# Kernel optimization log

Measured on AMD Instinct MI355X. Metric: run time of the kernel, lower is better.

Reference implementation:

```python
import jax, jax.numpy as jnp
import numpy as np

N_ENTS = 50000
N_RELS2 = 460  # num_rels * 2
H_DIM = 128
T = 8
E = 200000
M = 400000
RRELU_SLOPE = (1.0 / 8.0 + 1.0 / 3.0) / 2.0  # F.rrelu eval mode
EPS = 1e-12


def l2norm(x):
    # F.normalize(x) along last dim
    return x / jnp.maximum(jnp.linalg.norm(x, axis=-1, keepdims=True), EPS)


def gru_cell(x, h, W_ih, W_hh, b_ih, b_hh):
    # torch.nn.GRUCell math
    gi = x @ W_ih.T + b_ih
    gh = h @ W_hh.T + b_hh
    i_r, i_z, i_n = jnp.split(gi, 3, axis=-1)
    h_r, h_z, h_n = jnp.split(gh, 3, axis=-1)
    r = jax.nn.sigmoid(i_r + h_r)
    z = jax.nn.sigmoid(i_z + h_z)
    n = jnp.tanh(i_n + r * h_n)
    return (1.0 - z) * n + z * h


def rrelu(x):
    return jnp.where(x >= 0, x, RRELU_SLOPE * x)


def setup_inputs() -> dict:
    key = jax.random.key(0)
    ks = jax.random.split(key, 12)
    src = jax.random.randint(ks[0], (T, E), 0, N_ENTS, dtype=jnp.int32)
    dst = jax.random.randint(ks[1], (T, E), 0, N_ENTS, dtype=jnp.int32)
    etype = jax.random.randint(ks[2], (T, E), 0, N_RELS2, dtype=jnp.int32)
    r_to_e_idx = jax.random.randint(ks[3], (T, M), 0, N_ENTS, dtype=jnp.int32)
    rel_seg = jax.random.randint(ks[4], (T, M), 0, N_RELS2, dtype=jnp.int32)
    s = 1.0 / np.sqrt(H_DIM)
    dynamic_emb = jax.random.normal(ks[5], (N_ENTS, H_DIM), jnp.float32)
    emb_rel = jax.random.normal(ks[6], (N_RELS2, H_DIM), jnp.float32) * s
    gru_W_ih = jax.random.uniform(ks[7], (3 * H_DIM, 2 * H_DIM), jnp.float32, -s, s)
    gru_W_hh = jax.random.uniform(ks[8], (3 * H_DIM, H_DIM), jnp.float32, -s, s)
    gru_b_ih = jnp.zeros((3 * H_DIM,), jnp.float32)
    gru_b_hh = jnp.zeros((3 * H_DIM,), jnp.float32)
    rgcn_W = jax.random.normal(ks[9], (2, H_DIM, H_DIM), jnp.float32) * s  # 2 hidden layers
    time_gate_weight = jax.random.normal(ks[10], (H_DIM, H_DIM), jnp.float32) * s
    time_gate_bias = jnp.zeros((H_DIM,), jnp.float32)
    return {
        "src": src, "dst": dst, "etype": etype,
        "r_to_e_idx": r_to_e_idx, "rel_seg": rel_seg,
        "dynamic_emb": dynamic_emb, "emb_rel": emb_rel,
        "gru_W_ih": gru_W_ih, "gru_W_hh": gru_W_hh,
        "gru_b_ih": gru_b_ih, "gru_b_hh": gru_b_hh,
        "rgcn_W": rgcn_W,
        "time_gate_weight": time_gate_weight, "time_gate_bias": time_gate_bias,
    }


def reference(src, dst, etype, r_to_e_idx, rel_seg, dynamic_emb, emb_rel,
              gru_W_ih, gru_W_hh, gru_b_ih, gru_b_hh, rgcn_W,
              time_gate_weight, time_gate_bias):
    h_init = l2norm(dynamic_emb)  # layer_norm=True path

    def step(carry, xs):
        h, h0 = carry
        src_t, dst_t, etype_t, rte_t, rseg_t = xs
        # --- relation evolution: mean of incident entity embeddings per relation ---
        temp_e = h[rte_t]  # [M, d]
        sums = jax.ops.segment_sum(temp_e, rseg_t, num_segments=N_RELS2)
        cnts = jax.ops.segment_sum(jnp.ones((M,), h.dtype), rseg_t, num_segments=N_RELS2)
        x_mean = jnp.where(cnts[:, None] > 0, sums / jnp.maximum(cnts[:, None], 1.0), 0.0)
        x_input = jnp.concatenate([emb_rel, x_mean], axis=1)  # [2R, 2d]
        h0 = l2norm(gru_cell(x_input, h0, gru_W_ih, gru_W_hh, gru_b_ih, gru_b_hh))
        # --- RGCN (UnionRGCNLayer x2): msg=(h[src]+r[etype])@W, sum agg, 1/indeg norm, rrelu ---
        deg = jax.ops.segment_sum(jnp.ones((E,), h.dtype), dst_t, num_segments=N_ENTS)
        norm = jnp.where(deg > 0, 1.0 / jnp.maximum(deg, 1.0), 0.0)  # [N]
        nh = h
        for l in range(2):
            msg = (nh[src_t] + h0[etype_t]) @ rgcn_W[l]  # [E, d]
            agg = jax.ops.segment_sum(msg, dst_t, num_segments=N_ENTS) * norm[:, None]
            nh = rrelu(agg)
        current_h = l2norm(nh)
        # --- time gate fusion ---
        tw = jax.nn.sigmoid(h @ time_gate_weight + time_gate_bias)
        h_new = tw * current_h + (1.0 - tw) * h
        return (h_new, h0), h_new

    (_, h0_final), history = jax.lax.scan(
        step, (h_init, emb_rel), (src, dst, etype, r_to_e_idx, rel_seg))
    return history, h0_final  # [T, N, d], [2R, d]
```

## Files before the change

### kernel.cpp

```cpp
#include <hip/hip_runtime.h>
#include <math.h>

#define NENT 50000
#define NR2 460
#define HD 128
#define TS 8
#define EPC 200000
#define MPC 400000
#define RSLOPE 0.22916666666666666f
#define RBLK 128
#define NTOT (TS * NENT)
#define NB8 ((NTOT + 255) / 256)
#define SCAN2_PER ((NB8 + 255) / 256)
#define RSP 8

typedef __attribute__((ext_vector_type(8))) short bfrag;
typedef __attribute__((ext_vector_type(4))) float facc;

__device__ __forceinline__ float sigm(float x) { return 1.0f / (1.0f + expf(-x)); }
__device__ __forceinline__ float rrelu_f(float x) { return x >= 0.0f ? x : RSLOPE * x; }
__device__ __forceinline__ unsigned short f2bf_rne(float x) {
  unsigned u = __float_as_uint(x);
  unsigned r = (u + 0x7FFFu + ((u >> 16) & 1u)) >> 16;
  return (unsigned short)r;
}
__device__ __forceinline__ float bf2f(unsigned short b) {
  return __uint_as_float(((unsigned)b) << 16);
}
__device__ __forceinline__ float bfLO(unsigned u) { return __uint_as_float(u << 16); }
__device__ __forceinline__ float bfHI(unsigned u) { return __uint_as_float(u & 0xFFFF0000u); }

__global__ __launch_bounds__(HD) void k_l2rows(const float* __restrict__ in,
                                               float* __restrict__ out,
                                               unsigned short* __restrict__ out_bf) {
  int r = blockIdx.x, j = threadIdx.x;
  __shared__ float red[HD];
  float v = in[(size_t)r * HD + j];
  red[j] = v * v;
  __syncthreads();
  for (int s = HD / 2; s > 0; s >>= 1) { if (j < s) red[j] += red[j + s]; __syncthreads(); }
  float rn = 1.0f / fmaxf(sqrtf(red[0]), 1e-12f);
  float o = v * rn;
  out[(size_t)r * HD + j] = o;
  out_bf[(size_t)r * HD + j] = f2bf_rne(o);
}

__global__ void k_hist(const int* __restrict__ idx, int* __restrict__ cnt,
                       int n, int per_t, int stride) {
  int i = blockIdx.x * blockDim.x + threadIdx.x;
  int gs = gridDim.x * blockDim.x;
  for (; i < n; i += gs) atomicAdd(&cnt[(i / per_t) * stride + idx[i]], 1);
}

__global__ __launch_bounds__(256) void k_histR2(const int* __restrict__ rseg,
                                                int* __restrict__ blkcnt) {
  __shared__ int h[NR2];
  int b = blockIdx.x, t = blockIdx.y, tid = threadIdx.x;
  for (int i = tid; i < NR2; i += 256) h[i] = 0;
  __syncthreads();
  const int* rs = rseg + (size_t)t * MPC;
  int chunk = (MPC + RBLK - 1) / RBLK;
  int m0 = b * chunk, m1 = min(MPC, m0 + chunk);
  for (int m = m0 + tid; m < m1; m += 256) atomicAdd(&h[rs[m]], 1);
  __syncthreads();
  for (int i = tid; i < NR2; i += 256) blkcnt[((size_t)(t * RBLK + b)) * NR2 + i] = h[i];
}

__global__ __launch_bounds__(256) void k_scanR2a(const int* __restrict__ blkcnt,
                                                 int* __restrict__ tot) {
  int idx = blockIdx.x * 256 + threadIdx.x;
  if (idx >= TS * NR2) return;
  int t = idx / NR2, r = idx - t * NR2;
  int s = 0;
  for (int b = 0; b < RBLK; ++b) s += blkcnt[((size_t)(t * RBLK + b)) * NR2 + r];
  tot[idx] = s;
}

__global__ __launch_bounds__(512) void k_scanR2b(const int* __restrict__ tot,
    int* __restrict__ offsR, float* __restrict__ invc) {
  __shared__ int s[TS * NR2];
  int tid = threadIdx.x;
  for (int i = tid; i < TS * NR2; i += 512) s[i] = tot[i];
  __syncthreads();
  if (tid < TS) {
    int acc = tid * MPC;
    for (int r = 0; r < NR2; ++r) { int c = s[tid * NR2 + r]; s[tid * NR2 + r] = acc; acc += c; }
  }
  __syncthreads();
  for (int i = tid; i < TS * NR2; i += 512) {
    offsR[i] = s[i];
    int c = tot[i];
    invc[i] = c > 0 ? 1.0f / (float)c : 0.0f;
  }
  if (tid == 0) offsR[TS * NR2] = TS * MPC;
}

__global__ __launch_bounds__(256) void k_scanR2c(int* __restrict__ blkcnt,
                                                 const int* __restrict__ offsR) {
  int gw = (blockIdx.x * blockDim.x + threadIdx.x) >> 6;
  int lane = threadIdx.x & 63;
  if (gw >= TS * NR2) return;
  int t = gw / NR2, r = gw - t * NR2;
  size_t i0 = ((size_t)(t * RBLK + lane * 2)) * NR2 + r;
  size_t i1 = ((size_t)(t * RBLK + lane * 2 + 1)) * NR2 + r;
  int v0 = blkcnt[i0], v1 = blkcnt[i1];
  int s = v0 + v1;
  int sc = s;
  #pragma unroll
  for (int o = 1; o < 64; o <<= 1) {
    int x = __shfl_up(sc, o, 64);
    if (lane >= o) sc += x;
  }
  int basev = offsR[gw] + (sc - s);
  blkcnt[i0] = basev;
  blkcnt[i1] = basev + v0;
}

__global__ __launch_bounds__(256) void k_scatterR2(const int* __restrict__ rte,
    const int* __restrict__ rseg, const int* __restrict__ blkbase,
    int* __restrict__ out) {
  __shared__ int cur[NR2];
  int b = blockIdx.x, t = blockIdx.y, tid = threadIdx.x;
  for (int i = tid; i < NR2; i += 256) cur[i] = blkbase[((size_t)(t * RBLK + b)) * NR2 + i];
  __syncthreads();
  const int* rs = rseg + (size_t)t * MPC;
  const int* re = rte + (size_t)t * MPC;
  int chunk = (MPC + RBLK - 1) / RBLK;
  int m0 = b * chunk, m1 = min(MPC, m0 + chunk);
  for (int m = m0 + tid; m < m1; m += 256) {
    int r = rs[m];
    int p = atomicAdd(&cur[r], 1);
    out[p] = re[m];
  }
}

__global__ __launch_bounds__(256) void k_scan1(const int* __restrict__ deg,
    int* __restrict__ offs, float* __restrict__ normv, int* __restrict__ bsum) {
  __shared__ int sd[256];
  int b = blockIdx.x, tid = threadIdx.x;
  int i = b * 256 + tid;
  int v = (i < NTOT) ? deg[i] : 0;
  sd[tid] = v;
  __syncthreads();
  for (int o = 1; o < 256; o <<= 1) {
    int x = (tid >= o) ? sd[tid - o] : 0;
    __syncthreads();
    sd[tid] += x;
    __syncthreads();
  }
  if (i < NTOT) {
    offs[i] = sd[tid] - v;
    normv[i] = v > 0 ? 1.0f / (float)v : 0.0f;
  }
  if (tid == 255) bsum[b] = sd[255];
}

__global__ __launch_bounds__(256) void k_scan2(int* __restrict__ bsum) {
  __shared__ int part[256];
  int tid = threadIdx.x;
  int base = tid * SCAN2_PER;
  int local[SCAN2_PER];
  int s = 0;
  #pragma unroll
  for (int k = 0; k < SCAN2_PER; ++k) {
    int v = (base + k < NB8) ? bsum[base + k] : 0;
    local[k] = s;
    s += v;
  }
  part[tid] = s;
  __syncthreads();
  for (int o = 1; o < 256; o <<= 1) {
    int x = (tid >= o) ? part[tid - o] : 0;
    __syncthreads();
    part[tid] += x;
    __syncthreads();
  }
  int pre = (tid > 0) ? part[tid - 1] : 0;
  #pragma unroll
  for (int k = 0; k < SCAN2_PER; ++k)
    if (base + k < NB8) bsum[base + k] = pre + local[k];
}

__global__ __launch_bounds__(256) void k_scan3(int* __restrict__ offs, int* __restrict__ cur,
                                               const int* __restrict__ bsum) {
  int b = blockIdx.x;
  int i = b * 256 + threadIdx.x;
  if (i < NTOT) {
    int o = offs[i] + bsum[b];
    offs[i] = o;
    cur[i] = o;
  }
  if (b == 0 && threadIdx.x == 0) offs[NTOT] = TS * EPC;
}

__global__ void k_scatterE(const int* __restrict__ src, const int* __restrict__ dst,
                           const int* __restrict__ ety, int* __restrict__ cur,
                           unsigned* __restrict__ se) {
  int i = blockIdx.x * blockDim.x + threadIdx.x;
  int gs = gridDim.x * blockDim.x;
  for (; i < TS * EPC; i += gs) {
    int t = i / EPC;
    int d = dst[i];
    int p = atomicAdd(&cur[t * NENT + d], 1);
    se[p] = ((unsigned)src[i] << 9) | (unsigned)ety[i];
  }
}

__global__ __launch_bounds__(256) void k_prepW(const float* __restrict__ W,
    unsigned short* __restrict__ hi, unsigned short* __restrict__ lo) {
  int t = blockIdx.x * 256 + threadIdx.x;
  int nt = t >> 8, ks = (t >> 6) & 3, lane = t & 63;
  int n = nt * 16 + (lane & 15);
  int k0 = ks * 32 + ((lane >> 4) << 3);
  #pragma unroll
  for (int j = 0; j < 8; ++j) {
    float v = W[(k0 + j) * HD + n];
    unsigned short h = f2bf_rne(v);
    hi[t * 8 + j] = h;
    lo[t * 8 + j] = f2bf_rne(v - bf2f(h));
  }
}

__global__ __launch_bounds__(256) void k_relmean(const unsigned short* __restrict__ h_bf,
    const int* __restrict__ offs, const int* __restrict__ rte_csr,
    float* __restrict__ partials) {
  int rel = blockIdx.x, sp = blockIdx.y;
  int o0 = offs[rel], o1 = offs[rel + 1];
  int n = o1 - o0;
  int w = __builtin_amdgcn_readfirstlane(threadIdx.x >> 6);
  int lane = threadIdx.x & 63;
  int s0 = o0 + ((n * sp) >> 3);
  int s1 = o0 + ((n * (sp + 1)) >> 3);
  const unsigned* h4 = (const unsigned*)h_bf;
  float sx = 0.f, sy = 0.f;
  int p = s0 + w;
  for (; p + 12 < s1; p += 16) {
    int i0 = rte_csr[p];
    int i1 = rte_csr[p + 4];
    int i2 = rte_csr[p + 8];
    int i3 = rte_csr[p + 12];
    unsigned u0 = h4[(size_t)i0 * 64 + lane];
    unsigned u1 = h4[(size_t)i1 * 64 + lane];
    unsigned u2 = h4[(size_t)i2 * 64 + lane];
    unsigned u3 = h4[(size_t)i3 * 64 + lane];
    sx += (bfLO(u0) + bfLO(u1)) + (bfLO(u2) + bfLO(u3));
    sy += (bfHI(u0) + bfHI(u1)) + (bfHI(u2) + bfHI(u3));
  }
  for (; p < s1; p += 4) {
    unsigned u0 = h4[(size_t)rte_csr[p] * 64 + lane];
    sx += bfLO(u0);
    sy += bfHI(u0);
  }
  __shared__ float red[4][HD];
  red[w][lane * 2] = sx;
  red[w][lane * 2 + 1] = sy;
  __syncthreads();
  if (threadIdx.x < HD) {
    int j = threadIdx.x;
    float t = red[0][j] + red[1][j] + red[2][j] + red[3][j];
    partials[((size_t)sp * NR2 + rel) * HD + j] = t;
  }
}

__global__ __launch_bounds__(HD) void k_gru(
    const float* __restrict__ partials, const float* __restrict__ invcnt,
    const float* __restrict__ emb_rel, const float* __restrict__ h0s,
    const float* __restrict__ Wih, const float* __restrict__ Whh,
    const float* __restrict__ bih, const float* __restrict__ bhh,
    float* __restrict__ h0d) {
  int r = blockIdx.x, j = threadIdx.x;
  __shared__ __align__(16) float xr[2 * HD];
  __shared__ __align__(16) float hh[HD];
  __shared__ float red[HD];
  float inv = invcnt[r];
  xr[j] = emb_rel[r * HD + j];
  float xm = 0.f;
  #pragma unroll
  for (int sp = 0; sp < RSP; ++sp) xm += partials[((size_t)sp * NR2 + r) * HD + j];
  xr[HD + j] = xm * inv;
  float hv0 = h0s[r * HD + j];
  hh[j] = hv0;
  __syncthreads();
  float gr = bih[j], gz = bih[HD + j], gn = bih[2 * HD + j];
  const float4* W4 = (const float4*)Wih;
  int rowA = j * 64, rowB = (j + HD) * 64, rowC = (j + 2 * HD) * 64;
  #pragma unroll 4
  for (int k4 = 0; k4 < 64; ++k4) {
    float4 xa = ((const float4*)xr)[k4];
    float4 w0 = W4[rowA + k4];
    float4 w1 = W4[rowB + k4];
    float4 w2 = W4[rowC + k4];
    gr += w0.x * xa.x + w0.y * xa.y + w0.z * xa.z + w0.w * xa.w;
    gz += w1.x * xa.x + w1.y * xa.y + w1.z * xa.z + w1.w * xa.w;
    gn += w2.x * xa.x + w2.y * xa.y + w2.z * xa.z + w2.w * xa.w;
  }
  float hr = bhh[j], hz = bhh[HD + j], hn = bhh[2 * HD + j];
  const float4* Wh4 = (const float4*)Whh;
  int rA = j * 32, rB = (j + HD) * 32, rC = (j + 2 * HD) * 32;
  #pragma unroll 4
  for (int k4 = 0; k4 < 32; ++k4) {
    float4 xa = ((const float4*)hh)[k4];
    float4 w0 = Wh4[rA + k4];
    float4 w1 = Wh4[rB + k4];
    float4 w2 = Wh4[rC + k4];
    hr += w0.x * xa.x + w0.y * xa.y + w0.z * xa.z + w0.w * xa.w;
    hz += w1.x * xa.x + w1.y * xa.y + w1.z * xa.z + w1.w * xa.w;
    hn += w2.x * xa.x + w2.y * xa.y + w2.z * xa.z + w2.w * xa.w;
  }
  float rg = sigm(gr + hr);
  float zg = sigm(gz + hz);
  float ng = tanhf(gn + rg * hn);
  float hv = (1.0f - zg) * ng + zg * hv0;
  red[j] = hv * hv;
  __syncthreads();
  for (int s = HD / 2; s > 0; s >>= 1) { if (j < s) red[j] += red[j + s]; __syncthreads(); }
  float rn = 1.0f / fmaxf(sqrtf(red[0]), 1e-12f);
  h0d[r * HD + j] = hv * rn;
}

__global__ __launch_bounds__(256) void k_edge_csr(
    const unsigned short* __restrict__ nh_bf, const float* __restrict__ h0,
    const int* __restrict__ offs, const unsigned* __restrict__ se,
    const float* __restrict__ norm, float* __restrict__ agg) {
  int gw = __builtin_amdgcn_readfirstlane((blockIdx.x * blockDim.x + threadIdx.x) >> 6);
  int lane = threadIdx.x & 63;
  if (gw >= NENT) return;
  int o0 = offs[gw], o1 = offs[gw + 1];
  const unsigned* nh4 = (const unsigned*)nh_bf;
  const float2* h02 = (const float2*)h0;
  float sx = 0.f, sy = 0.f;
  int p = o0;
  for (; p + 4 <= o1; p += 4) {
    unsigned e0 = se[p], e1 = se[p + 1], e2 = se[p + 2], e3 = se[p + 3];
    unsigned ua = nh4[(size_t)(e0 >> 9) * 64 + lane];
    unsigned ub = nh4[(size_t)(e1 >> 9) * 64 + lane];
    unsigned uc = nh4[(size_t)(e2 >> 9) * 64 + lane];
    unsigned ud = nh4[(size_t)(e3 >> 9) * 64 + lane];
    float2 ra = h02[(size_t)(e0 & 511u) * 64 + lane];
    float2 rb = h02[(size_t)(e1 & 511u) * 64 + lane];
    float2 rc = h02[(size_t)(e2 & 511u) * 64 + lane];
    float2 rd = h02[(size_t)(e3 & 511u) * 64 + lane];
    sx += ((bfLO(ua) + ra.x) + (bfLO(ub) + rb.x)) +
          ((bfLO(uc) + rc.x) + (bfLO(ud) + rd.x));
    sy += ((bfHI(ua) + ra.y) + (bfHI(ub) + rb.y)) +
          ((bfHI(uc) + rc.y) + (bfHI(ud) + rd.y));
  }
  if (p + 2 <= o1) {
    unsigned e0 = se[p], e1 = se[p + 1];
    unsigned ua = nh4[(size_t)(e0 >> 9) * 64 + lane];
    unsigned ub = nh4[(size_t)(e1 >> 9) * 64 + lane];
    float2 ra = h02[(size_t)(e0 & 511u) * 64 + lane];
    float2 rb = h02[(size_t)(e1 & 511u) * 64 + lane];
    sx += (bfLO(ua) + ra.x) + (bfLO(ub) + rb.x);
    sy += (bfHI(ua) + ra.y) + (bfHI(ub) + rb.y);
    p += 2;
  }
  if (p < o1) {
    unsigned e0 = se[p];
    unsigned ua = nh4[(size_t)(e0 >> 9) * 64 + lane];
    float2 ra = h02[(size_t)(e0 & 511u) * 64 + lane];
    sx += bfLO(ua) + ra.x;
    sy += bfHI(ua) + ra.y;
  }
  float nm = norm[gw];
  ((float2*)agg)[(size_t)gw * 64 + lane] = make_float2(sx * nm, sy * nm);
}

__device__ __forceinline__ void stage_rows(const float* __restrict__ A, int base, int nrows,
                                           unsigned short* AsH, unsigned short* AsL,
                                           int tid) {
  const float4* A4 = (const float4*)A;
  #pragma unroll
  for (int it = 0; it < 8; ++it) {
    int idx = tid + it * 256;
    int r = idx >> 5, c4 = idx & 31;
    int c0 = c4 * 4;
    float4 v = make_float4(0.f, 0.f, 0.f, 0.f);
    if (base + r < nrows) v = A4[(size_t)(base + r) * 32 + c4];
    int chunk = (c0 >> 3) ^ (r & 7);
    int p = r * 128 + chunk * 8 + (c0 & 7);
    unsigned short h0 = f2bf_rne(v.x), h1 = f2bf_rne(v.y);
    unsigned short h2 = f2bf_rne(v.z), h3 = f2bf_rne(v.w);
    ushort4 hv; hv.x = h0; hv.y = h1; hv.z = h2; hv.w = h3;
    *(ushort4*)&AsH[p] = hv;
    ushort4 lv;
    lv.x = f2bf_rne(v.x - bf2f(h0)); lv.y = f2bf_rne(v.y - bf2f(h1));
    lv.z = f2bf_rne(v.z - bf2f(h2)); lv.w = f2bf_rne(v.w - bf2f(h3));
    *(ushort4*)&AsL[p] = lv;
  }
}

__device__ __forceinline__ void mfma_128(const unsigned short* AsH, const unsigned short* AsL,
                                         const unsigned short* __restrict__ wHi,
                                         const unsigned short* __restrict__ wLo,
                                         int w, int lane, facc* acc) {
  int lrow = lane & 15;
  int arow = w * 16 + lrow;
  #pragma unroll
  for (int ks = 0; ks < 4; ++ks) {
    int chunk = (ks * 4 + (lane >> 4)) ^ (arow & 7);
    int p = arow * 128 + chunk * 8;
    bfrag aH = *(const bfrag*)&AsH[p];
    bfrag aL = *(const bfrag*)&AsL[p];
    #pragma unroll
    for (int nt = 0; nt < 8; ++nt) {
      int fi = ((nt * 4 + ks) * 64 + lane) * 8;
      bfrag bH = *(const bfrag*)&wHi[fi];
      bfrag bL = *(const bfrag*)&wLo[fi];
      acc[nt] = __builtin_amdgcn_mfma_f32_16x16x32_bf16(aH, bH, acc[nt], 0, 0, 0);
      acc[nt] = __builtin_amdgcn_mfma_f32_16x16x32_bf16(aH, bL, acc[nt], 0, 0, 0);
      acc[nt] = __builtin_amdgcn_mfma_f32_16x16x32_bf16(aL, bH, acc[nt], 0, 0, 0);
    }
  }
}

__global__ __launch_bounds__(256) void k_mm1(
    const float* __restrict__ A, unsigned short* __restrict__ Abf,
    const unsigned short* __restrict__ wHi, const unsigned short* __restrict__ wLo,
    int nrows) {
  __shared__ __align__(16) unsigned short AsH[64 * 128];
  __shared__ __align__(16) unsigned short AsL[64 * 128];
  int tid = threadIdx.x;
  int base = blockIdx.x * 64;
  stage_rows(A, base, nrows, AsH, AsL, tid);
  __syncthreads();
  int w = tid >> 6, lane = tid & 63;
  int lrow = lane & 15, lk = lane >> 4;
  facc acc[8];
  #pragma unroll
  for (int nt = 0; nt < 8; ++nt) acc[nt] = (facc){0.f, 0.f, 0.f, 0.f};
  mfma_128(AsH, AsL, wHi, wLo, w, lane, acc);
  #pragma unroll
  for (int nt = 0; nt < 8; ++nt)
    #pragma unroll
    for (int r = 0; r < 4; ++r) {
      int row = base + w * 16 + lk * 4 + r;
      if (row < nrows) Abf[(size_t)row * HD + nt * 16 + lrow] = f2bf_rne(rrelu_f(acc[nt][r]));
    }
}

__global__ __launch_bounds__(256) void k_mm2_final(
    const float* __restrict__ A, const float* __restrict__ Hin,
    float* __restrict__ Hout, unsigned short* __restrict__ Hout_bf,
    const unsigned short* __restrict__ w2Hi, const unsigned short* __restrict__ w2Lo,
    const unsigned short* __restrict__ wtHi, const unsigned short* __restrict__ wtLo,
    const float* __restrict__ bias, int nrows) {
  __shared__ __align__(16) unsigned short AsH[64 * 128];
  __shared__ __align__(16) unsigned short AsL[64 * 128];
  int tid = threadIdx.x;
  int base = blockIdx.x * 64;
  int w = tid >> 6, lane = tid & 63;
  int lrow = lane & 15, lk = lane >> 4;
  stage_rows(A, base, nrows, AsH, AsL, tid);
  __syncthreads();
  facc acc[8];
  #pragma unroll
  for (int nt = 0; nt < 8; ++nt) acc[nt] = (facc){0.f, 0.f, 0.f, 0.f};
  mfma_128(AsH, AsL, w2Hi, w2Lo, w, lane, acc);
  #pragma unroll
  for (int nt = 0; nt < 8; ++nt)
    #pragma unroll
    for (int r = 0; r < 4; ++r) acc[nt][r] = rrelu_f(acc[nt][r]);
  __syncthreads();
  stage_rows(Hin, base, nrows, AsH, AsL, tid);
  __syncthreads();
  facc acc2[8];
  #pragma unroll
  for (int nt = 0; nt < 8; ++nt) acc2[nt] = (facc){0.f, 0.f, 0.f, 0.f};
  mfma_128(AsH, AsL, wtHi, wtLo, w, lane, acc2);
  float ss[4] = {0.f, 0.f, 0.f, 0.f};
  #pragma unroll
  for (int r = 0; r < 4; ++r) {
    #pragma unroll
    for (int nt = 0; nt < 8; ++nt) ss[r] += acc[nt][r] * acc[nt][r];
    #pragma unroll
    for (int o = 1; o < 16; o <<= 1) ss[r] += __shfl_xor(ss[r], o, 64);
    ss[r] = 1.0f / fmaxf(sqrtf(ss[r]), 1e-12f);
  }
  #pragma unroll
  for (int r = 0; r < 4; ++r) {
    int row = base + w * 16 + lk * 4 + r;
    if (row >= nrows) continue;
    #pragma unroll
    for (int nt = 0; nt < 8; ++nt) {
      int col = nt * 16 + lrow;
      float hv = Hin[(size_t)row * HD + col];
      float tw = sigm(acc2[nt][r] + bias[col]);
      float res = tw * (acc[nt][r] * ss[r]) + (1.0f - tw) * hv;
      Hout[(size_t)row * HD + col] = res;
      Hout_bf[(size_t)row * HD + col] = f2bf_rne(res);
    }
  }
}

extern "C" void kernel_launch(void* const* d_in, const int* in_sizes, int n_in,
                              void* d_out, int out_size, void* d_ws, size_t ws_size,
                              hipStream_t stream) {
  const int* src    = (const int*)d_in[0];
  const int* dst    = (const int*)d_in[1];
  const int* etype  = (const int*)d_in[2];
  const int* rte    = (const int*)d_in[3];
  const int* rseg   = (const int*)d_in[4];
  const float* dyn  = (const float*)d_in[5];
  const float* emb_rel = (const float*)d_in[6];
  const float* W_ih = (const float*)d_in[7];
  const float* W_hh = (const float*)d_in[8];
  const float* b_ih = (const float*)d_in[9];
  const float* b_hh = (const float*)d_in[10];
  const float* rgcnW = (const float*)d_in[11];
  const float* tgW  = (const float*)d_in[12];
  const float* tgB  = (const float*)d_in[13];
  float* out = (float*)d_out;
  (void)in_sizes; (void)n_in; (void)out_size; (void)ws_size;

  float* ws = (float*)d_ws;
  size_t off = 0;
  float* agg1    = ws + off; off += (size_t)NENT * HD;
  float* agg2    = ws + off; off += (size_t)NENT * HD;
  float* parts   = ws + off; off += (size_t)RSP * NR2 * HD;
  float* h0a     = ws + off; off += (size_t)NR2 * HD;
  float* h0b     = ws + off; off += (size_t)NR2 * HD;
  float* normv8  = ws + off; off += NTOT;
  float* invc8   = ws + off; off += TS * NR2;
  off = (off + 3) & ~(size_t)3;
  unsigned short* h_bf    = (unsigned short*)(ws + off); off += (size_t)NENT * HD / 2;
  unsigned short* agg1_bf = (unsigned short*)(ws + off); off += (size_t)NENT * HD / 2;
  unsigned short* wf = (unsigned short*)(ws + off);
  unsigned short* w1H = wf;            unsigned short* w1L = wf + 16384;
  unsigned short* w2H = wf + 32768;    unsigned short* w2L = wf + 49152;
  unsigned short* wtH = wf + 65536;    unsigned short* wtL = wf + 81920;
  off += (6 * 16384) / 2;
  unsigned* csr_se8 = (unsigned*)(ws + off); off += (size_t)TS * EPC;
  int* csr_rte8  = (int*)(ws + off);  off += (size_t)TS * MPC;
  int* degE8     = (int*)(ws + off);  off += NTOT;
  int* offsE8    = (int*)(ws + off);  off += NTOT + 2;
  int* curE8     = (int*)(ws + off);  off += NTOT;
  int* bsum      = (int*)(ws + off);  off += NB8;
  int* blkcntR8  = (int*)(ws + off);  off += (size_t)TS * RBLK * NR2;
  int* offsR8    = (int*)(ws + off);  off += TS * NR2 + 2;
  int* totR      = (int*)(ws + off);  off += TS * NR2;

  hipMemsetAsync(degE8, 0, (size_t)NTOT * sizeof(int), stream);
  k_hist<<<2048, 256, 0, stream>>>(dst, degE8, TS * EPC, EPC, NENT);
  k_scan1<<<NB8, 256, 0, stream>>>(degE8, offsE8, normv8, bsum);
  k_scan2<<<1, 256, 0, stream>>>(bsum);
  k_scan3<<<NB8, 256, 0, stream>>>(offsE8, curE8, bsum);
  k_scatterE<<<2048, 256, 0, stream>>>(src, dst, etype, curE8, csr_se8);
  k_histR2<<<dim3(RBLK, TS), 256, 0, stream>>>(rseg, blkcntR8);
  k_scanR2a<<<(TS * NR2 + 255) / 256, 256, 0, stream>>>(blkcntR8, totR);
  k_scanR2b<<<1, 512, 0, stream>>>(totR, offsR8, invc8);
  k_scanR2c<<<(TS * NR2 * 64 + 255) / 256, 256, 0, stream>>>(blkcntR8, offsR8);
  k_scatterR2<<<dim3(RBLK, TS), 256, 0, stream>>>(rte, rseg, blkcntR8, csr_rte8);
  k_prepW<<<8, 256, 0, stream>>>(rgcnW, w1H, w1L);
  k_prepW<<<8, 256, 0, stream>>>(rgcnW + HD * HD, w2H, w2L);
  k_prepW<<<8, 256, 0, stream>>>(tgW, wtH, wtL);

  k_l2rows<<<NENT, HD, 0, stream>>>(dyn, out, h_bf);

  float* h0bufs[2] = {h0a, h0b};
  for (int t = 0; t < TS; ++t) {
    const float* h = out + (size_t)(t == 0 ? 0 : (t - 1)) * NENT * HD;
    float* hout = out + (size_t)t * NENT * HD;
    const float* h0s = (t == 0) ? emb_rel : h0bufs[(t - 1) & 1];
    float* h0d = h0bufs[t & 1];

    k_relmean<<<dim3(NR2, RSP), 256, 0, stream>>>(h_bf, offsR8 + t * NR2, csr_rte8, parts);
    k_gru<<<NR2, HD, 0, stream>>>(parts, invc8 + t * NR2, emb_rel, h0s,
                                  W_ih, W_hh, b_ih, b_hh, h0d);

    k_edge_csr<<<(NENT * 64 + 255) / 256, 256, 0, stream>>>(
        h_bf, h0d, offsE8 + t * NENT, csr_se8, normv8 + t * NENT, agg1);
    k_mm1<<<(NENT + 63) / 64, 256, 0, stream>>>(agg1, agg1_bf, w1H, w1L, NENT);
    k_edge_csr<<<(NENT * 64 + 255) / 256, 256, 0, stream>>>(
        agg1_bf, h0d, offsE8 + t * NENT, csr_se8, normv8 + t * NENT, agg2);
    k_mm2_final<<<(NENT + 63) / 64, 256, 0, stream>>>(agg2, h, hout, h_bf,
                                                      w2H, w2L, wtH, wtL, tgB, NENT);
  }
  hipMemcpyAsync(out + (size_t)TS * NENT * HD, h0bufs[(TS - 1) & 1],
                 (size_t)NR2 * HD * sizeof(float), hipMemcpyDeviceToDevice, stream);
}
```

Measured before the change: 1.561 ms.

## Fuse relation mean with GRU, cache relation sums, and pair rows per wave in edge aggregation

Merges the relation-mean and GRU kernels into one 512-thread block per relation, which drops the partials buffer and one launch per step. The edge aggregation now has each wave process two destination rows so that more gathers are in flight. The first pass computes the per-node relation-embedding sum from a bf16 copy of h0 and stores it as bf16, and the second pass reuses that stored sum instead of gathering it again. The cost is bf16 rounding of h0 and of the cached sum, an imbalance when the two rows have different degrees, and a scatter kernel that now loops per timestep with a smaller grid.

```diff
diff --git a/kernel.cpp b/kernel.cpp
--- a/kernel.cpp
+++ b/kernel.cpp
@@ -2,6 +2,7 @@
 #include <math.h>
 
 #define NENT 50000
+#define NE2 (NENT / 2)
 #define NR2 460
 #define HD 128
 #define TS 8
@@ -12,7 +13,6 @@
 #define NTOT (TS * NENT)
 #define NB8 ((NTOT + 255) / 256)
 #define SCAN2_PER ((NB8 + 255) / 256)
-#define RSP 8
 
 typedef __attribute__((ext_vector_type(8))) short bfrag;
 typedef __attribute__((ext_vector_type(4))) float facc;
@@ -29,6 +29,9 @@
 }
 __device__ __forceinline__ float bfLO(unsigned u) { return __uint_as_float(u << 16); }
 __device__ __forceinline__ float bfHI(unsigned u) { return __uint_as_float(u & 0xFFFF0000u); }
+__device__ __forceinline__ unsigned packbf(float x, float y) {
+  return (unsigned)f2bf_rne(x) | ((unsigned)f2bf_rne(y) << 16);
+}
 
 __global__ __launch_bounds__(HD) void k_l2rows(const float* __restrict__ in,
                                                float* __restrict__ out,
@@ -196,13 +199,18 @@
 __global__ void k_scatterE(const int* __restrict__ src, const int* __restrict__ dst,
                            const int* __restrict__ ety, int* __restrict__ cur,
                            unsigned* __restrict__ se) {
-  int i = blockIdx.x * blockDim.x + threadIdx.x;
+  int tid0 = blockIdx.x * blockDim.x + threadIdx.x;
   int gs = gridDim.x * blockDim.x;
-  for (; i < TS * EPC; i += gs) {
-    int t = i / EPC;
-    int d = dst[i];
-    int p = atomicAdd(&cur[t * NENT + d], 1);
-    se[p] = ((unsigned)src[i] << 9) | (unsigned)ety[i];
+  for (int t = 0; t < TS; ++t) {
+    const int* s = src + (size_t)t * EPC;
+    const int* d = dst + (size_t)t * EPC;
+    const int* e = ety + (size_t)t * EPC;
+    int* ct = cur + t * NENT;
+    for (int i = tid0; i < EPC; i += gs) {
+      int dd = d[i];
+      int p = atomicAdd(&ct[dd], 1);
+      se[p] = ((unsigned)s[i] << 9) | (unsigned)e[i];
+    }
   }
 }
 
@@ -221,24 +229,27 @@
   }
 }
 
-__global__ __launch_bounds__(256) void k_relmean(const unsigned short* __restrict__ h_bf,
+__global__ __launch_bounds__(512) void k_relgru(
+    const unsigned short* __restrict__ h_bf,
     const int* __restrict__ offs, const int* __restrict__ rte_csr,
-    float* __restrict__ partials) {
-  int rel = blockIdx.x, sp = blockIdx.y;
+    const float* __restrict__ invcnt,
+    const float* __restrict__ emb_rel, const float* __restrict__ h0s,
+    const float* __restrict__ Wih, const float* __restrict__ Whh,
+    const float* __restrict__ bih, const float* __restrict__ bhh,
+    float* __restrict__ h0d, unsigned short* __restrict__ h0d_bf) {
+  int rel = blockIdx.x;
+  int tid = threadIdx.x;
+  int w = __builtin_amdgcn_readfirstlane(tid >> 6);
+  int lane = tid & 63;
   int o0 = offs[rel], o1 = offs[rel + 1];
   int n = o1 - o0;
-  int w = __builtin_amdgcn_readfirstlane(threadIdx.x >> 6);
-  int lane = threadIdx.x & 63;
-  int s0 = o0 + ((n * sp) >> 3);
-  int s1 = o0 + ((n * (sp + 1)) >> 3);
+  int s0 = o0 + ((n * w) >> 3);
+  int s1 = o0 + ((n * (w + 1)) >> 3);
   const unsigned* h4 = (const unsigned*)h_bf;
   float sx = 0.f, sy = 0.f;
-  int p = s0 + w;
-  for (; p + 12 < s1; p += 16) {
-    int i0 = rte_csr[p];
-    int i1 = rte_csr[p + 4];
-    int i2 = rte_csr[p + 8];
-    int i3 = rte_csr[p + 12];
+  int p = s0;
+  for (; p + 4 <= s1; p += 4) {
+    int i0 = rte_csr[p], i1 = rte_csr[p + 1], i2 = rte_csr[p + 2], i3 = rte_csr[p + 3];
     unsigned u0 = h4[(size_t)i0 * 64 + lane];
     unsigned u1 = h4[(size_t)i1 * 64 + lane];
     unsigned u2 = h4[(size_t)i2 * 64 + lane];
@@ -246,124 +257,162 @@
     sx += (bfLO(u0) + bfLO(u1)) + (bfLO(u2) + bfLO(u3));
     sy += (bfHI(u0) + bfHI(u1)) + (bfHI(u2) + bfHI(u3));
   }
-  for (; p < s1; p += 4) {
+  for (; p < s1; ++p) {
     unsigned u0 = h4[(size_t)rte_csr[p] * 64 + lane];
     sx += bfLO(u0);
     sy += bfHI(u0);
   }
-  __shared__ float red[4][HD];
+  __shared__ float red[8][HD];
   red[w][lane * 2] = sx;
   red[w][lane * 2 + 1] = sy;
   __syncthreads();
-  if (threadIdx.x < HD) {
-    int j = threadIdx.x;
-    float t = red[0][j] + red[1][j] + red[2][j] + red[3][j];
-    partials[((size_t)sp * NR2 + rel) * HD + j] = t;
-  }
-}
-
-__global__ __launch_bounds__(HD) void k_gru(
-    const float* __restrict__ partials, const float* __restrict__ invcnt,
-    const float* __restrict__ emb_rel, const float* __restrict__ h0s,
-    const float* __restrict__ Wih, const float* __restrict__ Whh,
-    const float* __restrict__ bih, const float* __restrict__ bhh,
-    float* __restrict__ h0d) {
-  int r = blockIdx.x, j = threadIdx.x;
   __shared__ __align__(16) float xr[2 * HD];
   __shared__ __align__(16) float hh[HD];
-  __shared__ float red[HD];
-  float inv = invcnt[r];
-  xr[j] = emb_rel[r * HD + j];
-  float xm = 0.f;
-  #pragma unroll
-  for (int sp = 0; sp < RSP; ++sp) xm += partials[((size_t)sp * NR2 + r) * HD + j];
-  xr[HD + j] = xm * inv;
-  float hv0 = h0s[r * HD + j];
-  hh[j] = hv0;
-  __syncthreads();
-  float gr = bih[j], gz = bih[HD + j], gn = bih[2 * HD + j];
-  const float4* W4 = (const float4*)Wih;
-  int rowA = j * 64, rowB = (j + HD) * 64, rowC = (j + 2 * HD) * 64;
-  #pragma unroll 4
-  for (int k4 = 0; k4 < 64; ++k4) {
-    float4 xa = ((const float4*)xr)[k4];
-    float4 w0 = W4[rowA + k4];
-    float4 w1 = W4[rowB + k4];
-    float4 w2 = W4[rowC + k4];
-    gr += w0.x * xa.x + w0.y * xa.y + w0.z * xa.z + w0.w * xa.w;
-    gz += w1.x * xa.x + w1.y * xa.y + w1.z * xa.z + w1.w * xa.w;
-    gn += w2.x * xa.x + w2.y * xa.y + w2.z * xa.z + w2.w * xa.w;
-  }
-  float hr = bhh[j], hz = bhh[HD + j], hn = bhh[2 * HD + j];
-  const float4* Wh4 = (const float4*)Whh;
-  int rA = j * 32, rB = (j + HD) * 32, rC = (j + 2 * HD) * 32;
-  #pragma unroll 4
-  for (int k4 = 0; k4 < 32; ++k4) {
-    float4 xa = ((const float4*)hh)[k4];
-    float4 w0 = Wh4[rA + k4];
-    float4 w1 = Wh4[rB + k4];
-    float4 w2 = Wh4[rC + k4];
-    hr += w0.x * xa.x + w0.y * xa.y + w0.z * xa.z + w0.w * xa.w;
-    hz += w1.x * xa.x + w1.y * xa.y + w1.z * xa.z + w1.w * xa.w;
-    hn += w2.x * xa.x + w2.y * xa.y + w2.z * xa.z + w2.w * xa.w;
-  }
-  float rg = sigm(gr + hr);
-  float zg = sigm(gz + hz);
-  float ng = tanhf(gn + rg * hn);
-  float hv = (1.0f - zg) * ng + zg * hv0;
-  red[j] = hv * hv;
-  __syncthreads();
-  for (int s = HD / 2; s > 0; s >>= 1) { if (j < s) red[j] += red[j + s]; __syncthreads(); }
-  float rn = 1.0f / fmaxf(sqrtf(red[0]), 1e-12f);
-  h0d[r * HD + j] = hv * rn;
-}
-
-__global__ __launch_bounds__(256) void k_edge_csr(
-    const unsigned short* __restrict__ nh_bf, const float* __restrict__ h0,
+  __shared__ float red2[HD];
+  float hv0 = 0.f;
+  if (tid < HD) {
+    int j = tid;
+    float inv = invcnt[rel];
+    float xm = 0.f;
+    #pragma unroll
+    for (int sp = 0; sp < 8; ++sp) xm += red[sp][j];
+    xr[j] = emb_rel[rel * HD + j];
+    xr[HD + j] = xm * inv;
+    hv0 = h0s[rel * HD + j];
+    hh[j] = hv0;
+  }
+  __syncthreads();
+  float hv = 0.f;
+  if (tid < HD) {
+    int j = tid;
+    float gr = bih[j], gz = bih[HD + j], gn = bih[2 * HD + j];
+    const float4* W4 = (const float4*)Wih;
+    int rowA = j * 64, rowB = (j + HD) * 64, rowC = (j + 2 * HD) * 64;
+    #pragma unroll 4
+    for (int k4 = 0; k4 < 64; ++k4) {
+      float4 xa = ((const float4*)xr)[k4];
+      float4 w0 = W4[rowA + k4];
+      float4 w1 = W4[rowB + k4];
+      float4 w2 = W4[rowC + k4];
+      gr += w0.x * xa.x + w0.y * xa.y + w0.z * xa.z + w0.w * xa.w;
+      gz += w1.x * xa.x + w1.y * xa.y + w1.z * xa.z + w1.w * xa.w;
+      gn += w2.x * xa.x + w2.y * xa.y + w2.z * xa.z + w2.w * xa.w;
+    }
+    float hr = bhh[j], hz = bhh[HD + j], hn = bhh[2 * HD + j];
+    const float4* Wh4 = (const float4*)Whh;
+    int rA = j * 32, rB = (j + HD) * 32, rC = (j + 2 * HD) * 32;
+    #pragma unroll 4
+    for (int k4 = 0; k4 < 32; ++k4) {
+      float4 xa = ((const float4*)hh)[k4];
+      float4 w0 = Wh4[rA + k4];
+      float4 w1 = Wh4[rB + k4];
+      float4 w2 = Wh4[rC + k4];
+      hr += w0.x * xa.x + w0.y * xa.y + w0.z * xa.z + w0.w * xa.w;
+      hz += w1.x * xa.x + w1.y * xa.y + w1.z * xa.z + w1.w * xa.w;
+      hn += w2.x * xa.x + w2.y * xa.y + w2.z * xa.z + w2.w * xa.w;
+    }
+    float rg = sigm(gr + hr);
+    float zg = sigm(gz + hz);
+    float ng = tanhf(gn + rg * hn);
+    hv = (1.0f - zg) * ng + zg * hv0;
+    red2[tid] = hv * hv;
+  }
+  __syncthreads();
+  for (int s = HD / 2; s > 0; s >>= 1) {
+    if (tid < s) red2[tid] += red2[tid + s];
+    __syncthreads();
+  }
+  if (tid < HD) {
+    float rn = 1.0f / fmaxf(sqrtf(red2[0]), 1e-12f);
+    float o = hv * rn;
+    h0d[rel * HD + tid] = o;
+    h0d_bf[rel * HD + tid] = f2bf_rne(o);
+  }
+}
+
+template<int PASS>
+__global__ __launch_bounds__(256) void k_edge2(
+    const unsigned short* __restrict__ nh_bf, const unsigned short* __restrict__ h0_bf,
     const int* __restrict__ offs, const unsigned* __restrict__ se,
-    const float* __restrict__ norm, float* __restrict__ agg) {
+    const float* __restrict__ norm, unsigned* __restrict__ Tbf,
+    float* __restrict__ agg) {
   int gw = __builtin_amdgcn_readfirstlane((blockIdx.x * blockDim.x + threadIdx.x) >> 6);
   int lane = threadIdx.x & 63;
-  if (gw >= NENT) return;
-  int o0 = offs[gw], o1 = offs[gw + 1];
+  if (gw >= NE2) return;
+  int rA = gw, rB = gw + NE2;
+  int a0 = offs[rA], a1 = offs[rA + 1];
+  int b0 = offs[rB], b1 = offs[rB + 1];
   const unsigned* nh4 = (const unsigned*)nh_bf;
-  const float2* h02 = (const float2*)h0;
-  float sx = 0.f, sy = 0.f;
-  int p = o0;
-  for (; p + 4 <= o1; p += 4) {
-    unsigned e0 = se[p], e1 = se[p + 1], e2 = se[p + 2], e3 = se[p + 3];
+  const unsigned* h04 = (const unsigned*)h0_bf;
+  float nax = 0.f, nay = 0.f, tax = 0.f, tay = 0.f;
+  float nbx = 0.f, nby = 0.f, tbx = 0.f, tby = 0.f;
+  int pa = a0, pb = b0;
+  for (; pa + 4 <= a1 && pb + 4 <= b1; pa += 4, pb += 4) {
+    unsigned e0 = se[pa], e1 = se[pa + 1], e2 = se[pa + 2], e3 = se[pa + 3];
+    unsigned f0 = se[pb], f1 = se[pb + 1], f2 = se[pb + 2], f3 = se[pb + 3];
     unsigned ua = nh4[(size_t)(e0 >> 9) * 64 + lane];
     unsigned ub = nh4[(size_t)(e1 >> 9) * 64 + lane];
     unsigned uc = nh4[(size_t)(e2 >> 9) * 64 + lane];
     unsigned ud = nh4[(size_t)(e3 >> 9) * 64 + lane];
-    float2 ra = h02[(size_t)(e0 & 511u) * 64 + lane];
-    float2 rb = h02[(size_t)(e1 & 511u) * 64 + lane];
-    float2 rc = h02[(size_t)(e2 & 511u) * 64 + lane];
-    float2 rd = h02[(size_t)(e3 & 511u) * 64 + lane];
-    sx += ((bfLO(ua) + ra.x) + (bfLO(ub) + rb.x)) +
-          ((bfLO(uc) + rc.x) + (bfLO(ud) + rd.x));
-    sy += ((bfHI(ua) + ra.y) + (bfHI(ub) + rb.y)) +
-          ((bfHI(uc) + rc.y) + (bfHI(ud) + rd.y));
-  }
-  if (p + 2 <= o1) {
-    unsigned e0 = se[p], e1 = se[p + 1];
+    unsigned va = nh4[(size_t)(f0 >> 9) * 64 + lane];
+    unsigned vb = nh4[(size_t)(f1 >> 9) * 64 + lane];
+    unsigned vc = nh4[(size_t)(f2 >> 9) * 64 + lane];
+    unsigned vd = nh4[(size_t)(f3 >> 9) * 64 + lane];
+    nax += (bfLO(ua) + bfLO(ub)) + (bfLO(uc) + bfLO(ud));
+    nay += (bfHI(ua) + bfHI(ub)) + (bfHI(uc) + bfHI(ud));
+    nbx += (bfLO(va) + bfLO(vb)) + (bfLO(vc) + bfLO(vd));
+    nby += (bfHI(va) + bfHI(vb)) + (bfHI(vc) + bfHI(vd));
+    if (PASS == 1) {
+      unsigned ha = h04[(size_t)(e0 & 511u) * 64 + lane];
+      unsigned hb = h04[(size_t)(e1 & 511u) * 64 + lane];
+      unsigned hc = h04[(size_t)(e2 & 511u) * 64 + lane];
+      unsigned hd = h04[(size_t)(e3 & 511u) * 64 + lane];
+      unsigned ga = h04[(size_t)(f0 & 511u) * 64 + lane];
+      unsigned gb = h04[(size_t)(f1 & 511u) * 64 + lane];
+      unsigned gc = h04[(size_t)(f2 & 511u) * 64 + lane];
+      unsigned gd = h04[(size_t)(f3 & 511u) * 64 + lane];
+      tax += (bfLO(ha) + bfLO(hb)) + (bfLO(hc) + bfLO(hd));
+      tay += (bfHI(ha) + bfHI(hb)) + (bfHI(hc) + bfHI(hd));
+      tbx += (bfLO(ga) + bfLO(gb)) + (bfLO(gc) + bfLO(gd));
+      tby += (bfHI(ga) + bfHI(gb)) + (bfHI(gc) + bfHI(gd));
+    }
+  }
+  for (; pa < a1; ++pa) {
+    unsigned e0 = se[pa];
     unsigned ua = nh4[(size_t)(e0 >> 9) * 64 + lane];
-    unsigned ub = nh4[(size_t)(e1 >> 9) * 64 + lane];
-    float2 ra = h02[(size_t)(e0 & 511u) * 64 + lane];
-    float2 rb = h02[(size_t)(e1 & 511u) * 64 + lane];
-    sx += (bfLO(ua) + ra.x) + (bfLO(ub) + rb.x);
-    sy += (bfHI(ua) + ra.y) + (bfHI(ub) + rb.y);
-    p += 2;
-  }
-  if (p < o1) {
-    unsigned e0 = se[p];
-    unsigned ua = nh4[(size_t)(e0 >> 9) * 64 + lane];
-    float2 ra = h02[(size_t)(e0 & 511u) * 64 + lane];
-    sx += bfLO(ua) + ra.x;
-    sy += bfHI(ua) + ra.y;
-  }
-  float nm = norm[gw];
-  ((float2*)agg)[(size_t)gw * 64 + lane] = make_float2(sx * nm, sy * nm);
+    nax += bfLO(ua);
+    nay += bfHI(ua);
+    if (PASS == 1) {
+      unsigned ha = h04[(size_t)(e0 & 511u) * 64 + lane];
+      tax += bfLO(ha);
+      tay += bfHI(ha);
+    }
+  }
+  for (; pb < b1; ++pb) {
+    unsigned f0 = se[pb];
+    unsigned va = nh4[(size_t)(f0 >> 9) * 64 + lane];
+    nbx += bfLO(va);
+    nby += bfHI(va);
+    if (PASS == 1) {
+      unsigned ga = h04[(size_t)(f0 & 511u) * 64 + lane];
+      tbx += bfLO(ga);
+      tby += bfHI(ga);
+    }
+  }
+  float nma = norm[rA], nmb = norm[rB];
+  if (PASS == 1) {
+    Tbf[(size_t)rA * 64 + lane] = packbf(tax, tay);
+    Tbf[(size_t)rB * 64 + lane] = packbf(tbx, tby);
+    ((float2*)agg)[(size_t)rA * 64 + lane] = make_float2((nax + tax) * nma, (nay + tay) * nma);
+    ((float2*)agg)[(size_t)rB * 64 + lane] = make_float2((nbx + tbx) * nmb, (nby + tby) * nmb);
+  } else {
+    unsigned tva = Tbf[(size_t)rA * 64 + lane];
+    unsigned tvb = Tbf[(size_t)rB * 64 + lane];
+    ((float2*)agg)[(size_t)rA * 64 + lane] =
+        make_float2((nax + bfLO(tva)) * nma, (nay + bfHI(tva)) * nma);
+    ((float2*)agg)[(size_t)rB * 64 + lane] =
+        make_float2((nbx + bfLO(tvb)) * nmb, (nby + bfHI(tvb)) * nmb);
+  }
 }
 
 __device__ __forceinline__ void stage_rows(const float* __restrict__ A, int base, int nrows,
@@ -517,14 +566,16 @@
   size_t off = 0;
   float* agg1    = ws + off; off += (size_t)NENT * HD;
   float* agg2    = ws + off; off += (size_t)NENT * HD;
-  float* parts   = ws + off; off += (size_t)RSP * NR2 * HD;
   float* h0a     = ws + off; off += (size_t)NR2 * HD;
   float* h0b     = ws + off; off += (size_t)NR2 * HD;
   float* normv8  = ws + off; off += NTOT;
   float* invc8   = ws + off; off += TS * NR2;
   off = (off + 3) & ~(size_t)3;
+  unsigned* Tbf  = (unsigned*)(ws + off); off += (size_t)NENT * 64;
   unsigned short* h_bf    = (unsigned short*)(ws + off); off += (size_t)NENT * HD / 2;
   unsigned short* agg1_bf = (unsigned short*)(ws + off); off += (size_t)NENT * HD / 2;
+  unsigned short* h0abf   = (unsigned short*)(ws + off); off += (size_t)NR2 * HD / 2 + 1;
+  unsigned short* h0bbf   = (unsigned short*)(ws + off); off += (size_t)NR2 * HD / 2 + 1;
   unsigned short* wf = (unsigned short*)(ws + off);
   unsigned short* w1H = wf;            unsigned short* w1L = wf + 16384;
   unsigned short* w2H = wf + 32768;    unsigned short* w2L = wf + 49152;
@@ -545,7 +596,7 @@
   k_scan1<<<NB8, 256, 0, stream>>>(degE8, offsE8, normv8, bsum);
   k_scan2<<<1, 256, 0, stream>>>(bsum);
   k_scan3<<<NB8, 256, 0, stream>>>(offsE8, curE8, bsum);
-  k_scatterE<<<2048, 256, 0, stream>>>(src, dst, etype, curE8, csr_se8);
+  k_scatterE<<<1024, 256, 0, stream>>>(src, dst, etype, curE8, csr_se8);
   k_histR2<<<dim3(RBLK, TS), 256, 0, stream>>>(rseg, blkcntR8);
   k_scanR2a<<<(TS * NR2 + 255) / 256, 256, 0, stream>>>(blkcntR8, totR);
   k_scanR2b<<<1, 512, 0, stream>>>(totR, offsR8, invc8);
@@ -558,21 +609,24 @@
   k_l2rows<<<NENT, HD, 0, stream>>>(dyn, out, h_bf);
 
   float* h0bufs[2] = {h0a, h0b};
+  unsigned short* h0bfbufs[2] = {h0abf, h0bbf};
   for (int t = 0; t < TS; ++t) {
     const float* h = out + (size_t)(t == 0 ? 0 : (t - 1)) * NENT * HD;
     float* hout = out + (size_t)t * NENT * HD;
     const float* h0s = (t == 0) ? emb_rel : h0bufs[(t - 1) & 1];
     float* h0d = h0bufs[t & 1];
-
-    k_relmean<<<dim3(NR2, RSP), 256, 0, stream>>>(h_bf, offsR8 + t * NR2, csr_rte8, parts);
-    k_gru<<<NR2, HD, 0, stream>>>(parts, invc8 + t * NR2, emb_rel, h0s,
-                                  W_ih, W_hh, b_ih, b_hh, h0d);
-
-    k_edge_csr<<<(NENT * 64 + 255) / 256, 256, 0, stream>>>(
-        h_bf, h0d, offsE8 + t * NENT, csr_se8, normv8 + t * NENT, agg1);
+    unsigned short* h0d_bf = h0bfbufs[t & 1];
+
+    k_relgru<<<NR2, 512, 0, stream>>>(h_bf, offsR8 + t * NR2, csr_rte8,
+                                      invc8 + t * NR2, emb_rel, h0s,
+                                      W_ih, W_hh, b_ih, b_hh, h0d, h0d_bf);
+
+    k_edge2<1><<<(NE2 * 64 + 255) / 256, 256, 0, stream>>>(
+        h_bf, h0d_bf, offsE8 + t * NENT, csr_se8, normv8 + t * NENT, Tbf, agg1);
     k_mm1<<<(NENT + 63) / 64, 256, 0, stream>>>(agg1, agg1_bf, w1H, w1L, NENT);
-    k_edge_csr<<<(NENT * 64 + 255) / 256, 256, 0, stream>>>(
-        agg1_bf, h0d, offsE8 + t * NENT, csr_se8, normv8 + t * NENT, agg2);
+    k_edge2<2><<<(NE2 * 64 + 255) / 256, 256, 0, stream>>>(
+        agg1_bf, (const unsigned short*)nullptr, offsE8 + t * NENT, csr_se8,
+        normv8 + t * NENT, Tbf, agg2);
     k_mm2_final<<<(NENT + 63) / 64, 256, 0, stream>>>(agg2, h, hout, h_bf,
                                                       w2H, w2L, wtH, wtL, tgB, NENT);
   }
```

Result: slower. 1.595 ms (+2.2%).
